# Optimization experiments

Measured on AMD Instinct MI355X. Metric: run time of the kernel, lower is better.

## Reference

```python
import jax, jax.numpy as jnp
import numpy as np
import math

D_MODEL = 512
NUM_HEADS = 8
B, L = 2, 4096
EPS_NORM = 1e-8
PLASTICITY = 1.0


def setup_inputs() -> dict:
    key = jax.random.key(0)
    ks = jax.random.split(key, 6)
    D, H = D_MODEL, NUM_HEADS
    std = 1.0 / math.sqrt(D)
    x = jax.random.normal(ks[0], (B, L, D), dtype=jnp.float32)
    qkv_w = jax.random.normal(ks[1], (3 * D, D), dtype=jnp.float32) * std
    qkv_b = jnp.zeros((3 * D,), dtype=jnp.float32)
    out_w = jax.random.normal(ks[2], (D, D), dtype=jnp.float32) * std
    out_b = jnp.zeros((D,), dtype=jnp.float32)
    decay_w = jax.random.normal(ks[3], (H, D), dtype=jnp.float32) * 0.02
    decay_b = jnp.full((H,), 4.0, dtype=jnp.float32)
    norm_scale = jnp.ones((D,), dtype=jnp.float32)
    return {"x": x, "qkv_w": qkv_w, "qkv_b": qkv_b, "out_w": out_w,
            "out_b": out_b, "decay_w": decay_w, "decay_b": decay_b,
            "norm_scale": norm_scale}


def _hebbian_forward(x, qkv_w, qkv_b, out_w, out_b, decay_w, decay_b, norm_scale):
    Bsz, Lsz, D = x.shape
    H = NUM_HEADS
    E = D // H
    # QKV projection (torch Linear: y = x @ W.T + b)
    qkv = x @ qkv_w.T + qkv_b
    q, k, v = jnp.split(qkv, 3, axis=-1)
    q = q.reshape(Bsz, Lsz, H, E)
    k = k.reshape(Bsz, Lsz, H, E)
    v = v.reshape(Bsz, Lsz, H, E)
    # feature map: elu(x) + 1
    q = (jax.nn.elu(q) + 1.0) / math.sqrt(E)
    k = jax.nn.elu(k) + 1.0
    # input-dependent decay per head
    decay_logits = x @ decay_w.T + decay_b          # (B,L,H)
    lambdas = (0.9 + 0.1 * jax.nn.sigmoid(decay_logits)) * PLASTICITY
    log_lambdas = jnp.log(jnp.clip(lambdas, 1e-6))[..., None]   # (B,L,H,1)
    log_lambda_cum = jnp.clip(jnp.cumsum(log_lambdas, axis=1), -50.0, 50.0)
    decay_k = jnp.exp(-log_lambda_cum)
    decay_q = jnp.exp(log_lambda_cum)
    k_decayed = k * decay_k
    q_decayed = q * decay_q
    # outer-product memory state cumsum: (B,L,H,E,E)
    kv = jnp.einsum('blhe,blhf->blhef', k_decayed, v)
    memory_state = jnp.cumsum(kv, axis=1)
    k_sum_decayed = jnp.cumsum(k_decayed, axis=1)
    num = jnp.einsum('blhe,blhef->blhf', q_decayed, memory_state)
    den = jnp.einsum('blhe,blhe->blh', q_decayed, k_sum_decayed)[..., None] + 1e-6
    out = (num / den).reshape(Bsz, Lsz, D)
    out = out @ out_w.T + out_b
    # RMSNorm (dropout is identity in eval)
    rnorm = jax.lax.rsqrt(jnp.mean(out * out, axis=-1, keepdims=True) + EPS_NORM)
    return out * rnorm * norm_scale


def reference(x, qkv_w, qkv_b, out_w, out_b, decay_w, decay_b, norm_scale):
    return _hebbian_forward(x, qkv_w, qkv_b, out_w, out_b, decay_w, decay_b, norm_scale)
```

## Files before the change

kernel.cpp:

```cpp
#include <hip/hip_runtime.h>

typedef unsigned short u16;
typedef unsigned int u32;

#define B_ 2
#define L_ 4096
#define D_ 512
#define H_ 8
#define E_ 64
#define M_ (B_*L_)
#define TD (3*D_)
#define NCH (L_/64)
#define BH (B_*H_)

typedef short bf16x8 __attribute__((ext_vector_type(8)));
typedef float f32x4 __attribute__((ext_vector_type(4)));

__device__ __forceinline__ float bf2f(u16 u){ return __uint_as_float(((u32)u)<<16); }
__device__ __forceinline__ u16 f2bf(float f){
  u32 u = __float_as_uint(f);
  u32 r = u + 0x7FFFu + ((u>>16)&1u);
  return (u16)(r>>16);
}
__device__ __forceinline__ float elu1(float v){ return v>0.f ? v+1.f : __expf(v); }

__device__ __forceinline__ void async_ld16(const u16* g, u16* l){
  __builtin_amdgcn_global_load_lds(
      (const __attribute__((address_space(1))) void*)g,
      (__attribute__((address_space(3))) void*)l, 16, 0, 0);
}

__global__ __launch_bounds__(256) void decay_conv_kernel(const float* __restrict__ x,
    const float* __restrict__ dw, const float* __restrict__ db,
    const float* __restrict__ qw, const float* __restrict__ ow,
    float* __restrict__ ll, u16* __restrict__ xb,
    u16* __restrict__ qwb, u16* __restrict__ owb)
{
  int blk = blockIdx.x;
  if (blk < 2048){
    int wv = threadIdx.x>>6, lane = threadIdx.x&63;
    int m = blk*4 + wv;
    float xr[8];
    #pragma unroll
    for (int i=0;i<8;i++) xr[i] = x[(size_t)m*D_ + lane + 64*i];
    #pragma unroll
    for (int i=0;i<8;i++) xb[(size_t)m*D_ + lane + 64*i] = f2bf(xr[i]);
    int b = m >> 12, l = m & (L_-1);
    float acc8[8];
    #pragma unroll
    for (int h=0; h<8; h++){
      float a = 0.f;
      #pragma unroll
      for (int i=0;i<8;i++) a += xr[i]*dw[h*D_ + lane + 64*i];
      acc8[h] = a;
    }
    float s4[4];
    #pragma unroll
    for (int i=0;i<4;i++){
      float a = acc8[2*i], bb = acc8[2*i+1];
      bool odd = lane & 1;
      float keep = odd ? bb : a;
      float send = odd ? a : bb;
      s4[i] = keep + __shfl_xor(send, 1);
    }
    float s2[2];
    #pragma unroll
    for (int j=0;j<2;j++){
      float a = s4[2*j], bb = s4[2*j+1];
      bool sel = (lane>>1) & 1;
      float keep = sel ? bb : a;
      float send = sel ? a : bb;
      s2[j] = keep + __shfl_xor(send, 2);
    }
    float r;
    {
      bool sel = (lane>>2) & 1;
      float keep = sel ? s2[1] : s2[0];
      float send = sel ? s2[0] : s2[1];
      r = keep + __shfl_xor(send, 4);
    }
    r += __shfl_xor(r, 8);
    r += __shfl_xor(r, 16);
    r += __shfl_xor(r, 32);
    if (lane < 8){
      float z = r + db[lane];
      float lam = 0.9f + 0.1f/(1.f + __expf(-z));
      ll[((b*H_+lane)*L_) + l] = __logf(lam);
    }
  } else {
    int gid = (blk-2048)*256 + threadIdx.x;
    const float* src; u16* dst; int off;
    if (gid < 196608){ src = qw; dst = qwb; off = gid; }
    else { src = ow; dst = owb; off = gid - 196608; }
    float4 v = ((const float4*)src)[off];
    ushort4 o; o.x=f2bf(v.x); o.y=f2bf(v.y); o.z=f2bf(v.z); o.w=f2bf(v.w);
    ((ushort4*)dst)[off] = o;
  }
}

__global__ __launch_bounds__(256) void scan_kernel(const float* __restrict__ ll,
    float* __restrict__ cb)
{
  int bh = blockIdx.x, t = threadIdx.x;
  int lane = t & 63, wv = t >> 6;
  const float* p = ll + (size_t)bh*L_ + t*16;
  float s[16];
  #pragma unroll
  for (int q=0;q<4;q++){
    float4 v = *(const float4*)(p + q*4);
    s[q*4+0]=v.x; s[q*4+1]=v.y; s[q*4+2]=v.z; s[q*4+3]=v.w;
  }
  #pragma unroll
  for (int i=1;i<16;i++) s[i] += s[i-1];
  float tot = s[15];
  float ws = tot;
  #pragma unroll
  for (int off=1; off<64; off<<=1){
    float tmp = __shfl_up(ws, off);
    if (lane >= off) ws += tmp;
  }
  __shared__ float wsum[4];
  if (lane == 63) wsum[wv] = ws;
  __syncthreads();
  float base = 0.f;
  #pragma unroll
  for (int w2=0; w2<3; w2++) if (w2 < wv) base += wsum[w2];
  float ex = base + ws - tot;
  float* c = cb + (size_t)bh*L_ + t*16;
  #pragma unroll
  for (int i=0;i<16;i++) c[i] = fminf(50.f, fmaxf(-50.f, ex + s[i]));
}

__global__ __launch_bounds__(256) void gemm_qkv_fused(const u16* __restrict__ A,
    const u16* __restrict__ W, const float* __restrict__ bias,
    const float* __restrict__ cb,
    u16* __restrict__ qc, u16* __restrict__ kc, u16* __restrict__ vc)
{
  __shared__ u16 SM[17408];
  u16* As0 = SM;
  u16* Bs0 = SM + 8192;
  const int K = 512;
  int n0 = blockIdx.x*128, m0 = blockIdx.y*128;
  int t = threadIdx.x, wave = t>>6, lane = t&63;
  int wm = (wave>>1)*64, wn = (wave&1)*64;
  f32x4 acc[4][4] = {};
  int srow = wave*32 + (lane>>2);
  int scol = (lane&3)*8;
  const u16* gA = A + (size_t)(m0+srow)*K + scol;
  const u16* gB = W + (size_t)(n0+srow)*K + scol;
  int q8 = (lane>>4)*8, r16 = lane&15;
  {
    u16* lA = As0 + wave*1024;
    u16* lB = Bs0 + wave*1024;
    async_ld16(gA,                lA);
    async_ld16(gA + 16*(size_t)K, lA + 512);
    async_ld16(gB,                lB);
    async_ld16(gB + 16*(size_t)K, lB + 512);
  }
  __syncthreads();
  int cur = 0;
  #pragma unroll 2
  for (int k0=0; k0<K; k0+=32){
    if (k0 + 32 < K){
      u16* lA = As0 + (cur^1)*4096 + wave*1024;
      u16* lB = Bs0 + (cur^1)*4096 + wave*1024;
      async_ld16(gA + k0+32,                lA);
      async_ld16(gA + k0+32 + 16*(size_t)K, lA + 512);
      async_ld16(gB + k0+32,                lB);
      async_ld16(gB + k0+32 + 16*(size_t)K, lB + 512);
    }
    bf16x8 af[4], bfr[4];
    #pragma unroll
    for (int i=0;i<4;i++) af[i]  = *(const bf16x8*)&As0[cur*4096 + (wm + i*16 + r16)*32 + q8];
    #pragma unroll
    for (int j=0;j<4;j++) bfr[j] = *(const bf16x8*)&Bs0[cur*4096 + (wn + j*16 + r16)*32 + q8];
    #pragma unroll
    for (int i=0;i<4;i++)
      #pragma unroll
      for (int j=0;j<4;j++)
        acc[i][j] = __builtin_amdgcn_mfma_f32_16x16x32_bf16(af[i], bfr[j], acc[i][j], 0,0,0);
    __syncthreads();
    cur ^= 1;
  }
  int g = lane>>4;
  #pragma unroll
  for (int j=0;j<4;j++){
    int col = wn + j*16 + r16;
    float bv = bias[n0 + col];
    #pragma unroll
    for (int i=0;i<4;i++){
      int rbase = wm + i*16 + g*4;
      #pragma unroll
      for (int r=0;r<4;r++)
        SM[(rbase+r)*136 + col] = f2bf(acc[i][j][r] + bv);
    }
  }
  __syncthreads();
  int sec = n0 >> 9;
  #pragma unroll
  for (int u=0;u<8;u++){
    int idx = t + 256*u;
    int rloc = idx >> 4;
    int colg = (idx & 15) * 8;
    int row = m0 + rloc;
    int nn = (n0 + colg) & 511;
    int h2 = nn>>6, e0 = nn&63;
    int bh2 = ((row>>12)<<3) | h2;
    int bid = (bh2<<6) | ((row>>6)&63);
    int l6 = row & 63;
    union { uint4 v; u16 s[8]; } dat;
    dat.v = *(const uint4*)&SM[rloc*136 + colg];
    size_t a = ((size_t)(bid*2 + (e0>>5)))*2048 + (size_t)l6*32 + (e0&31);
    if (sec == 0){
      float eqc = __expf(cb[((size_t)bh2<<12) | (row & 4095)])*0.125f;
      #pragma unroll
      for (int jj=0;jj<8;jj++) dat.s[jj] = f2bf(elu1(bf2f(dat.s[jj]))*eqc);
      *(uint4*)(qc + a) = dat.v;
    } else if (sec == 1){
      float ekc = __expf(-cb[((size_t)bh2<<12) | (row & 4095)]);
      #pragma unroll
      for (int jj=0;jj<8;jj++) dat.s[jj] = f2bf(elu1(bf2f(dat.s[jj]))*ekc);
      *(uint4*)(kc + a) = dat.v;
    } else {
      *(uint4*)(vc + a) = dat.v;
    }
  }
}

__global__ __launch_bounds__(256) void chunk_sums_kernel(const u16* __restrict__ kc,
    const u16* __restrict__ vc, u16* __restrict__ Stc, float* __restrict__ ksc)
{
  int bid = blockIdx.x;
  __shared__ u16 Kc[4096], Vc[4096];
  __shared__ u16 Ktl[5120], Vtl[5120];
  __shared__ float ksr[256];
  int t = threadIdx.x, w = t>>6, lane = t&63;
  {
    const u16* gk = kc + (size_t)bid*4096 + w*1024 + lane*8;
    const u16* gv = vc + (size_t)bid*4096 + w*1024 + lane*8;
    async_ld16(gk,       Kc + w*1024);
    async_ld16(gk + 512, Kc + w*1024 + 512);
    async_ld16(gv,       Vc + w*1024);
    async_ld16(gv + 512, Vc + w*1024 + 512);
  }
  __syncthreads();
  int e = t & 63, jq = t >> 6;
  {
    u16 kv[16] __attribute__((aligned(16)));
    u16 vv[16] __attribute__((aligned(16)));
    float ksum = 0.f;
    #pragma unroll
    for (int jj=0;jj<16;jj++){
      int j = jq*16+jj;
      kv[jj] = Kc[(e>>5)*2048 + j*32 + (e&31)];
      ksum += bf2f(kv[jj]);
      vv[jj] = Vc[(e>>5)*2048 + j*32 + (e&31)];
    }
    int kh2 = jq>>1, jl = (jq&1)*16;
    u16* kt = &Ktl[(kh2*64 + e)*40 + jl];
    u16* vt = &Vtl[(kh2*64 + e)*40 + jl];
    *(uint4*)kt     = *(const uint4*)&kv[0];
    *(uint4*)(kt+8) = *(const uint4*)&kv[8];
    *(uint4*)vt     = *(const uint4*)&vv[0];
    *(uint4*)(vt+8) = *(const uint4*)&vv[8];
    ksr[t] = ksum;
  }
  __syncthreads();
  int r16 = lane & 15, q8 = (lane>>4)*8;
  bf16x8 av[2];
  #pragma unroll
  for (int kh=0;kh<2;kh++)
    av[kh] = *(const bf16x8*)&Vtl[(kh*64 + w*16 + r16)*40 + q8];
  f32x4 acc[4] = {};
  #pragma unroll
  for (int et=0;et<4;et++)
    #pragma unroll
    for (int kh=0;kh<2;kh++){
      bf16x8 bv = *(const bf16x8*)&Ktl[(kh*64 + et*16 + r16)*40 + q8];
      acc[et] = __builtin_amdgcn_mfma_f32_16x16x32_bf16(av[kh], bv, acc[et], 0,0,0);
    }
  #pragma unroll
  for (int et=0;et<4;et++){
    int eh = et>>1, el = (et&1)*16 + r16;
    #pragma unroll
    for (int r=0;r<4;r++){
      int f = w*16 + (lane>>4)*4 + r;
      Stc[((size_t)bid*2 + eh)*2048 + f*32 + el] = f2bf(acc[et][r]);
    }
  }
  if (t < 64) ksc[bid*64 + t] = ksr[t] + ksr[64+t] + ksr[128+t] + ksr[192+t];
}

__global__ __launch_bounds__(256) void chunk_prefix_kernel(u16* __restrict__ Stc,
    float* __restrict__ ksc)
{
  int blk = blockIdx.x, t = threadIdx.x;
  if (blk < 128){
    int gid = blk*256 + t;
    int bh = gid >> 11, e2 = gid & 2047;
    u32* p = (u32*)Stc + (size_t)bh*131072 + e2;
    float r0 = 0.f, r1 = 0.f;
    #pragma unroll 16
    for (int ch=0; ch<NCH; ch++){
      u32 v = p[ch*2048];
      float lo = bf2f((u16)(v & 0xffffu));
      float hi = bf2f((u16)(v >> 16));
      p[ch*2048] = (u32)f2bf(r0) | ((u32)f2bf(r1) << 16);
      r0 += lo; r1 += hi;
    }
  } else {
    int gid2 = (blk-128)*256 + t;
    int bh2 = gid2 >> 6, e = gid2 & 63;
    float* kp = ksc + bh2*4096 + e;
    float kr = 0.f;
    #pragma unroll 8
    for (int ch=0; ch<NCH; ch++){
      float v = kp[ch*64]; kp[ch*64] = kr; kr += v;
    }
  }
}

__global__ __launch_bounds__(256) void chunk_out_kernel(const u16* __restrict__ qc,
    const u16* __restrict__ kc, const u16* __restrict__ vc,
    const u16* __restrict__ Stc, const float* __restrict__ ksc,
    u16* __restrict__ attn)
{
  int bid = blockIdx.x;
  int bh = bid >> 6, ch = bid & 63;
  int b = bh >> 3, h = bh & 7;
  __shared__ u16 Kb_l[4096];
  __shared__ u16 Vc_l[4096];
  __shared__ u16 St_l[4096];
  __shared__ u16 Vt[5120];
  __shared__ u16 Ab[4096];
  __shared__ float R2[320];
  int t = threadIdx.x, w = t>>6, lane = t&63;
  size_t mbase = (size_t)b*L_ + ch*64;
  {
    const u16* gk = kc  + (size_t)bid*4096 + w*1024 + lane*8;
    const u16* gv = vc  + (size_t)bid*4096 + w*1024 + lane*8;
    const u16* gs = Stc + (size_t)bid*4096 + w*1024 + lane*8;
    async_ld16(gk,       Kb_l + w*1024);
    async_ld16(gk + 512, Kb_l + w*1024 + 512);
    async_ld16(gv,       Vc_l + w*1024);
    async_ld16(gv + 512, Vc_l + w*1024 + 512);
    async_ld16(gs,       St_l + w*1024);
    async_ld16(gs + 512, St_l + w*1024 + 512);
  }
  int r16 = lane & 15, q8 = (lane>>4)*8;
  const u16* qg = qc + (size_t)bid*4096;
  bf16x8 aq[2];
  #pragma unroll
  for (int eh=0;eh<2;eh++)
    aq[eh] = *(const bf16x8*)(qg + eh*2048 + (w*16 + r16)*32 + q8);
  int l4 = t>>2, q4 = t&3;
  int ehd = q4>>1, el0 = (q4&1)*16;
  bf16x8 x1 = *(const bf16x8*)(qg + ehd*2048 + l4*32 + el0);
  bf16x8 x2 = *(const bf16x8*)(qg + ehd*2048 + l4*32 + el0 + 8);
  union { float4 v[4]; float f[16]; } kp;
  #pragma unroll
  for (int qq=0;qq<4;qq++)
    kp.v[qq] = *(const float4*)(ksc + bid*64 + q4*16 + qq*4);
  __syncthreads();
  {
    int e = t & 63, jq = t >> 6;
    u16 vv[16] __attribute__((aligned(16)));
    #pragma unroll
    for (int jj=0;jj<16;jj++)
      vv[jj] = Vc_l[(e>>5)*2048 + (jq*16+jj)*32 + (e&31)];
    int jh = jq>>1, jl = (jq&1)*16;
    u16* vt = &Vt[(jh*64 + e)*40 + jl];
    *(uint4*)vt     = *(const uint4*)&vv[0];
    *(uint4*)(vt+8) = *(const uint4*)&vv[8];
  }
  f32x4 accA[4] = {};
  #pragma unroll
  for (int jt=0;jt<4;jt++)
    #pragma unroll
    for (int eh=0;eh<2;eh++){
      bf16x8 bv = *(const bf16x8*)&Kb_l[(eh*64 + jt*16 + r16)*32 + q8];
      accA[jt] = __builtin_amdgcn_mfma_f32_16x16x32_bf16(aq[eh], bv, accA[jt], 0,0,0);
    }
  float dkp = 0.f;
  #pragma unroll
  for (int i=0;i<8;i++)
    dkp += bf2f((u16)x1[i])*kp.f[i] + bf2f((u16)x2[i])*kp.f[8+i];
  #pragma unroll
  for (int jt=0;jt<4;jt++)
    #pragma unroll
    for (int r=0;r<4;r++){
      int lr = w*16 + ((lane>>4)<<2) + r;
      int j  = jt*16 + r16;
      Ab[((jt>>1)*64 + lr)*32 + (jt&1)*16 + r16] = (j <= lr) ? f2bf(accA[jt][r]) : (u16)0;
    }
  __syncthreads();
  float dA = 0.f;
  {
    int jh2 = q4>>1, jl0 = (q4&1)*16;
    bf16x8 y1 = *(const bf16x8*)&Ab[(jh2*64 + l4)*32 + jl0];
    bf16x8 y2 = *(const bf16x8*)&Ab[(jh2*64 + l4)*32 + jl0 + 8];
    #pragma unroll
    for (int i=0;i<8;i++) dA += bf2f((u16)y1[i]) + bf2f((u16)y2[i]);
  }
  R2[t] = dkp + dA;
  __syncthreads();
  if (t < 64) R2[256+t] = R2[t*4] + R2[t*4+1] + R2[t*4+2] + R2[t*4+3] + 1e-6f;
  bf16x8 aA[2];
  #pragma unroll
  for (int jh=0;jh<2;jh++)
    aA[jh] = *(const bf16x8*)&Ab[(jh*64 + w*16 + r16)*32 + q8];
  f32x4 acc[4] = {};
  #pragma unroll
  for (int ft=0;ft<4;ft++){
    #pragma unroll
    for (int jh=0;jh<2;jh++){
      bf16x8 bv = *(const bf16x8*)&Vt[(jh*64 + ft*16 + r16)*40 + q8];
      acc[ft] = __builtin_amdgcn_mfma_f32_16x16x32_bf16(aA[jh], bv, acc[ft], 0,0,0);
    }
    #pragma unroll
    for (int eh=0;eh<2;eh++){
      bf16x8 bv = *(const bf16x8*)&St_l[(eh*64 + ft*16 + r16)*32 + q8];
      acc[ft] = __builtin_amdgcn_mfma_f32_16x16x32_bf16(aq[eh], bv, acc[ft], 0,0,0);
    }
  }
  __syncthreads();
  float inv[4];
  #pragma unroll
  for (int r=0;r<4;r++) inv[r] = 1.f / R2[256 + w*16 + ((lane>>4)<<2) + r];
  #pragma unroll
  for (int ft=0;ft<4;ft++)
    #pragma unroll
    for (int r=0;r<4;r++){
      int lr = w*16 + ((lane>>4)<<2) + r;
      attn[(mbase + lr)*D_ + h*64 + ft*16 + r16] = f2bf(acc[ft][r]*inv[r]);
    }
}

__global__ __launch_bounds__(256) void gemm_rms_kernel(const u16* __restrict__ A,
    const u16* __restrict__ W, const float* __restrict__ bias,
    const float* __restrict__ gnorm, float* __restrict__ out)
{
  __shared__ u16 As[2][32*32];
  __shared__ u16 Bs[2][512*32];
  __shared__ float ssq_l[4][32];
  __shared__ float rinv_l[32];
  int m0 = blockIdx.x*32;
  int t = threadIdx.x, wave = t>>6, lane = t&63;
  int wn = wave*128;
  int r16 = lane&15, q8 = (lane>>4)*8;
  f32x4 acc[2][8] = {};
  int scol = (t&3)*8;
  const u16* gB = W + (size_t)(t>>2)*512 + scol;
  const u16* gA = A + (size_t)(m0 + (t>>2))*512 + scol;
  {
    if (wave < 2) async_ld16(gA, As[0] + wave*512);
    #pragma unroll
    for (int it=0; it<8; it++)
      async_ld16(gB + it*32768, Bs[0] + wave*512 + it*2048);
  }
  __syncthreads();
  int cur = 0;
  #pragma unroll 2
  for (int k0=0; k0<512; k0+=32){
    if (k0 < 480){
      if (wave < 2) async_ld16(gA + k0+32, As[cur^1] + wave*512);
      #pragma unroll
      for (int it=0; it<8; it++)
        async_ld16(gB + k0+32 + it*32768, Bs[cur^1] + wave*512 + it*2048);
    }
    bf16x8 af0 = *(const bf16x8*)&As[cur][r16*32 + q8];
    bf16x8 af1 = *(const bf16x8*)&As[cur][(16 + r16)*32 + q8];
    #pragma unroll
    for (int j=0;j<8;j++){
      bf16x8 bv = *(const bf16x8*)&Bs[cur][(wn + j*16 + r16)*32 + q8];
      acc[0][j] = __builtin_amdgcn_mfma_f32_16x16x32_bf16(af0, bv, acc[0][j], 0,0,0);
      acc[1][j] = __builtin_amdgcn_mfma_f32_16x16x32_bf16(af1, bv, acc[1][j], 0,0,0);
    }
    __syncthreads();
    cur ^= 1;
  }
  int g = lane>>4;
  float bv8[8], gv8[8];
  #pragma unroll
  for (int j=0;j<8;j++){ int col = wn + j*16 + r16; bv8[j] = bias[col]; gv8[j] = gnorm[col]; }
  float ssq[2][4] = {};
  #pragma unroll
  for (int i=0;i<2;i++)
    #pragma unroll
    for (int j=0;j<8;j++)
      #pragma unroll
      for (int r=0;r<4;r++){
        float v = acc[i][j][r] + bv8[j];
        acc[i][j][r] = v;
        ssq[i][r] += v*v;
      }
  #pragma unroll
  for (int off=1; off<16; off<<=1)
    #pragma unroll
    for (int i=0;i<2;i++)
      #pragma unroll
      for (int r=0;r<4;r++)
        ssq[i][r] += __shfl_xor(ssq[i][r], off);
  if (r16 == 0){
    #pragma unroll
    for (int i=0;i<2;i++)
      #pragma unroll
      for (int r=0;r<4;r++)
        ssq_l[wave][i*16 + g*4 + r] = ssq[i][r];
  }
  __syncthreads();
  if (t < 32)
    rinv_l[t] = rsqrtf((ssq_l[0][t]+ssq_l[1][t]+ssq_l[2][t]+ssq_l[3][t])*(1.f/512.f) + 1e-8f);
  __syncthreads();
  #pragma unroll
  for (int i=0;i<2;i++)
    #pragma unroll
    for (int r=0;r<4;r++){
      int row = m0 + i*16 + g*4 + r;
      float ri = rinv_l[i*16 + g*4 + r];
      #pragma unroll
      for (int j=0;j<8;j++)
        out[(size_t)row*512 + wn + j*16 + r16] = acc[i][j][r]*ri*gv8[j];
    }
}

extern "C" void kernel_launch(void* const* d_in, const int* in_sizes, int n_in,
                              void* d_out, int out_size, void* d_ws, size_t ws_size,
                              hipStream_t stream)
{
  const float* x     = (const float*)d_in[0];
  const float* w_qkv = (const float*)d_in[1];
  const float* b_qkv = (const float*)d_in[2];
  const float* w_out = (const float*)d_in[3];
  const float* b_out = (const float*)d_in[4];
  const float* w_dec = (const float*)d_in[5];
  const float* b_dec = (const float*)d_in[6];
  const float* gnorm = (const float*)d_in[7];
  float* out = (float*)d_out;

  char* ws = (char*)d_ws;
  u16*   qc   = (u16*)(ws);
  u16*   kc   = (u16*)(ws + 8388608);
  u16*   vc   = (u16*)(ws + 16777216);
  u16*   Stc  = (u16*)(ws + 25165824);
  float* ksc  = (float*)(ws + 33554432);
  float* ll   = (float*)(ws + 33816576);
  float* cb   = (float*)(ws + 34078720);
  u16*   xb   = (u16*)(ws + 34340864);
  u16*   qwb  = (u16*)(ws + 42729472);
  u16*   owb  = (u16*)(ws + 44302336);
  u16*   attn = xb;

  decay_conv_kernel<<<dim3(3072), dim3(256), 0, stream>>>(x, w_dec, b_dec, w_qkv, w_out,
                                                          ll, xb, qwb, owb);
  scan_kernel<<<dim3(BH), dim3(256), 0, stream>>>(ll, cb);
  gemm_qkv_fused<<<dim3(TD/128, M_/128), dim3(256), 0, stream>>>(xb, qwb, b_qkv, cb, qc, kc, vc);
  chunk_sums_kernel<<<dim3(BH*NCH), dim3(256), 0, stream>>>(kc, vc, Stc, ksc);
  chunk_prefix_kernel<<<dim3(132), dim3(256), 0, stream>>>(Stc, ksc);
  chunk_out_kernel<<<dim3(BH*NCH), dim3(256), 0, stream>>>(qc, kc, vc, Stc, ksc, attn);
  gemm_rms_kernel<<<dim3(M_/32), dim3(256), 0, stream>>>(attn, owb, b_out, gnorm, out);
}
```

Measured before the change: 154.4 us.

## Triple-buffer QKV GEMM loads and use a single partial-wait barrier per k-step

The QKV GEMM moves from double to triple-buffered LDS staging, with two k-tiles prefetched ahead and a partial vmcnt wait, so that global-to-LDS copies overlap more with MFMA work and each iteration needs only one barrier. The output GEMM+RMS kernel moves its barrier to the top of the loop, using an explicit vmcnt(0) wait plus s_barrier instead of a trailing __syncthreads. The cost is more LDS per block in the QKV GEMM, which may lower occupancy, and the hand-written waitcnt counts depend on how the async loads are issued.

```diff
diff --git a/kernel.cpp b/kernel.cpp
--- a/kernel.cpp
+++ b/kernel.cpp
@@ -136,9 +136,7 @@
     const float* __restrict__ cb,
     u16* __restrict__ qc, u16* __restrict__ kc, u16* __restrict__ vc)
 {
-  __shared__ u16 SM[17408];
-  u16* As0 = SM;
-  u16* Bs0 = SM + 8192;
+  __shared__ u16 SM[24576];
   const int K = 512;
   int n0 = blockIdx.x*128, m0 = blockIdx.y*128;
   int t = threadIdx.x, wave = t>>6, lane = t&63;
@@ -149,39 +147,35 @@
   const u16* gA = A + (size_t)(m0+srow)*K + scol;
   const u16* gB = W + (size_t)(n0+srow)*K + scol;
   int q8 = (lane>>4)*8, r16 = lane&15;
-  {
-    u16* lA = As0 + wave*1024;
-    u16* lB = Bs0 + wave*1024;
-    async_ld16(gA,                lA);
-    async_ld16(gA + 16*(size_t)K, lA + 512);
-    async_ld16(gB,                lB);
-    async_ld16(gB + 16*(size_t)K, lB + 512);
-  }
-  __syncthreads();
-  int cur = 0;
-  #pragma unroll 2
+  auto STAGE = [&](u16* buf, int k0){
+    u16* lA = buf + wave*1024;
+    u16* lB = buf + 4096 + wave*1024;
+    async_ld16(gA + k0,                lA);
+    async_ld16(gA + k0 + 16*(size_t)K, lA + 512);
+    async_ld16(gB + k0,                lB);
+    async_ld16(gB + k0 + 16*(size_t)K, lB + 512);
+  };
+  u16 *cB = SM, *nB = SM + 8192, *tB = SM + 16384;
+  STAGE(cB, 0);
+  STAGE(nB, 32);
   for (int k0=0; k0<K; k0+=32){
-    if (k0 + 32 < K){
-      u16* lA = As0 + (cur^1)*4096 + wave*1024;
-      u16* lB = Bs0 + (cur^1)*4096 + wave*1024;
-      async_ld16(gA + k0+32,                lA);
-      async_ld16(gA + k0+32 + 16*(size_t)K, lA + 512);
-      async_ld16(gB + k0+32,                lB);
-      async_ld16(gB + k0+32 + 16*(size_t)K, lB + 512);
-    }
+    if (k0 + 32 < K) asm volatile("s_waitcnt vmcnt(4)" ::: "memory");
+    else             asm volatile("s_waitcnt vmcnt(0)" ::: "memory");
+    __builtin_amdgcn_s_barrier();
+    if (k0 + 64 < K) STAGE(tB, k0 + 64);
     bf16x8 af[4], bfr[4];
     #pragma unroll
-    for (int i=0;i<4;i++) af[i]  = *(const bf16x8*)&As0[cur*4096 + (wm + i*16 + r16)*32 + q8];
-    #pragma unroll
-    for (int j=0;j<4;j++) bfr[j] = *(const bf16x8*)&Bs0[cur*4096 + (wn + j*16 + r16)*32 + q8];
+    for (int i=0;i<4;i++) af[i]  = *(const bf16x8*)&cB[(wm + i*16 + r16)*32 + q8];
+    #pragma unroll
+    for (int j=0;j<4;j++) bfr[j] = *(const bf16x8*)&cB[4096 + (wn + j*16 + r16)*32 + q8];
     #pragma unroll
     for (int i=0;i<4;i++)
       #pragma unroll
       for (int j=0;j<4;j++)
         acc[i][j] = __builtin_amdgcn_mfma_f32_16x16x32_bf16(af[i], bfr[j], acc[i][j], 0,0,0);
-    __syncthreads();
-    cur ^= 1;
-  }
+    u16* tmp = cB; cB = nB; nB = tB; tB = tmp;
+  }
+  __syncthreads();
   int g = lane>>4;
   #pragma unroll
   for (int j=0;j<4;j++){
@@ -440,8 +434,8 @@
     const u16* __restrict__ W, const float* __restrict__ bias,
     const float* __restrict__ gnorm, float* __restrict__ out)
 {
-  __shared__ u16 As[2][32*32];
-  __shared__ u16 Bs[2][512*32];
+  __shared__ u16 As[2][1024];
+  __shared__ u16 Bs[2][16384];
   __shared__ float ssq_l[4][32];
   __shared__ float rinv_l[32];
   int m0 = blockIdx.x*32;
@@ -458,10 +452,10 @@
     for (int it=0; it<8; it++)
       async_ld16(gB + it*32768, Bs[0] + wave*512 + it*2048);
   }
-  __syncthreads();
   int cur = 0;
-  #pragma unroll 2
   for (int k0=0; k0<512; k0+=32){
+    asm volatile("s_waitcnt vmcnt(0)" ::: "memory");
+    __builtin_amdgcn_s_barrier();
     if (k0 < 480){
       if (wave < 2) async_ld16(gA + k0+32, As[cur^1] + wave*512);
       #pragma unroll
@@ -476,7 +470,6 @@
       acc[0][j] = __builtin_amdgcn_mfma_f32_16x16x32_bf16(af0, bv, acc[0][j], 0,0,0);
       acc[1][j] = __builtin_amdgcn_mfma_f32_16x16x32_bf16(af1, bv, acc[1][j], 0,0,0);
     }
-    __syncthreads();
     cur ^= 1;
   }
   int g = lane>>4;
```

Result: no change. 152.5 us (-1.2%).
